# Kernel tuning notes

Measured on AMD Instinct MI355X. Metric: run time of the kernel, lower is better.

## Reference

```python
import jax, jax.numpy as jnp
import numpy as np

B, N, M, V, H, K = 32, 9, 128, 512, 256, 8
TYPES, PAD, TAU = 21, 0, 1.0
NS, NT = N - 1, TYPES - 9  # span slots (2..N), type slots (9..TYPES-1)


def setup_inputs() -> dict:
    key = jax.random.key(0)
    ks = jax.random.split(key, 6)
    decodings = jax.random.normal(ks[0], (B, N, M, V), jnp.float32)
    target_types = jax.random.randint(ks[1], (B,), 9, TYPES)
    spans = jax.random.randint(ks[2], (B,), 2, N + 1)
    type_emb = jax.random.normal(ks[3], (TYPES, H), jnp.float32)
    dec_sem_W = jax.random.normal(ks[4], (NS, NT, K * (N + 1), H), jnp.float32) / np.sqrt(H).astype(np.float32)
    dec_sem_b = jnp.zeros((NS, NT, K * (N + 1)), jnp.float32)
    u = jax.random.uniform(ks[5], (B, K, N + 1), jnp.float32, 1e-10, 1.0)
    gumbel = -jnp.log(-jnp.log(u))
    return dict(decodings=decodings, type_emb=type_emb, dec_sem_W=dec_sem_W,
                dec_sem_b=dec_sem_b, gumbel=gumbel,
                target_types=target_types, spans=spans)


def reference(decodings, type_emb, dec_sem_W, dec_sem_b, gumbel, target_types, spans):
    # --- per-sample template logits: decoder_sem[span-2][type-9](type_embedding) ---
    emb = type_emb[target_types]                           # (B, H)
    Wi = dec_sem_W[spans - 2, target_types - 9]            # (B, K*(N+1), H)
    bi = dec_sem_b[spans - 2, target_types - 9]            # (B, K*(N+1))
    logits = (jnp.einsum('boh,bh->bo', Wi, emb) + bi).reshape(B, K, N + 1)
    pos = jnp.arange(N + 1)
    valid = pos[None, None, :] <= spans[:, None, None]     # first span+1 slots only
    logits = jnp.where(valid, logits, -1e30)
    logp = jax.nn.log_softmax(logits, -1)
    # gumbel_softmax(hard=True), straight-through
    y_soft = jax.nn.softmax((logp + gumbel) / TAU, -1)
    y_hard = jax.nn.one_hot(jnp.argmax(y_soft, -1), N + 1, dtype=y_soft.dtype)
    dt = y_hard + y_soft - jax.lax.stop_gradient(y_soft)
    dt = jnp.where(valid, dt, 0.0)
    # type == 20 uses the fixed start template (row 0 picks decoding 0, rest pad)
    start = jnp.zeros((K, N + 1)).at[0, 1].set(1.0).at[1:, 0].set(1.0)
    dt = jnp.where((target_types == 20)[:, None, None], start[None], dt)

    # --- apply_decoder_template, vectorized over batch ---
    pad_row = jnp.tile(jax.nn.one_hot(PAD, V, dtype=decodings.dtype), M)  # (M*V,)
    pos_m = jnp.arange(M)

    def per_sample(dt_i, dec_i):
        choices = jnp.concatenate([pad_row[None], dec_i.reshape(N, M * V)], 0)  # (N+1, M*V)
        out = (dt_i @ choices).reshape(K, M, V)            # (K, M, V)
        idxs = jnp.argmax(out, -1)                         # (K, M)
        raw_len = jnp.max(jnp.where(idxs != PAD, pos_m + 1, 0), axis=1)  # (K,)
        ends = jnp.minimum(jnp.cumsum(raw_len), M)
        starts = jnp.concatenate([jnp.zeros(1, ends.dtype), ends[:-1]])
        lens = ends - starts                               # sequential clipped concat
        dest = starts[:, None] + pos_m[None]
        ok = pos_m[None] < lens[:, None]
        dest = jnp.where(ok, dest, M)                      # dump invalid writes in row M
        res = jnp.zeros((M + 1, V), out.dtype).at[dest.reshape(-1)].add(
            out.reshape(K * M, V) * ok.reshape(-1, 1))
        return res[:M]

    new_d = jax.vmap(per_sample)(dt, decodings)            # (B, M, V)
    new_v = jnp.zeros((B, 20, 3, V), decodings.dtype)
    return new_d, new_v
```

## Files before the change

### kernel.cpp

```cpp
#include <hip/hip_runtime.h>

#define B 32
#define N 9
#define M 128
#define V 512
#define H 256
#define K 8
#define NT 12
#define NP1 10
#define SPLITS 4
#define ROWS_PER_SPLIT 32
#define NEWV_ROWS (B*20*3)

__device__ __forceinline__ float wave_sum(float v) {
    #pragma unroll
    for (int off = 32; off > 0; off >>= 1) v += __shfl_xor(v, off, 64);
    return v;
}

__global__ __launch_bounds__(256) void k_sel_rawlen(
    const float* __restrict__ dec, const float* __restrict__ type_emb,
    const float* __restrict__ W, const float* __restrict__ bias,
    const float* __restrict__ gumbel, const int* __restrict__ types,
    const int* __restrict__ spans,
    int* __restrict__ jstar, int* __restrict__ part)
{
    const int blk = blockIdx.x;
    const int s  = blk & (SPLITS - 1);
    const int bk = blk >> 2;
    const int b  = bk >> 3, k = bk & 7;
    const int t = threadIdx.x, wave = t >> 6, lane = t & 63;

    __shared__ float logits_s[NP1];
    __shared__ int   j_s;
    __shared__ int   best_s[4];

    if (wave == 0) {
        const int typ  = types[b];
        const int span = spans[b];
        const long base = ((long)(span - 2) * NT + (typ - 9)) * (K * NP1) + k * NP1;
        const float e0 = type_emb[typ * H + lane      ];
        const float e1 = type_emb[typ * H + lane +  64];
        const float e2 = type_emb[typ * H + lane + 128];
        const float e3 = type_emb[typ * H + lane + 192];
        #pragma unroll
        for (int j = 0; j < NP1; ++j) {
            const float* w = W + (base + j) * H;
            float ssum = w[lane      ] * e0 + w[lane +  64] * e1
                       + w[lane + 128] * e2 + w[lane + 192] * e3;
            ssum = wave_sum(ssum);
            if (lane == 0) logits_s[j] = ssum;
        }
        if (lane == 0) {
            int bj = 0;
            if (typ == 20) {
                bj = (k == 0) ? 1 : 0;
            } else {
                float bestv = -3.0e38f;
                for (int j = 0; j <= span; ++j) {
                    float v = logits_s[j] + bias[base + j] + gumbel[bk * NP1 + j];
                    if (v > bestv) { bestv = v; bj = j; }
                }
            }
            j_s = bj;
        }
    }
    __syncthreads();
    const int j = j_s;
    if (t == 0) jstar[bk] = j;

    int best = 0;
    if (j > 0) {
        const float* src = dec + ((long)(b * N + (j - 1)) * M) * V;
        const int m0 = s * ROWS_PER_SPLIT + wave * 8;
        #pragma unroll
        for (int i = 0; i < 8; ++i) {
            const int m = m0 + i;
            const float4* row = (const float4*)(src + (long)m * V);
            float4 a = row[lane];
            float4 c = row[lane + 64];
            float x0 = __shfl(a.x, 0, 64);
            float loc = (lane == 0) ? fmaxf(fmaxf(a.y, a.z), a.w)
                                    : fmaxf(fmaxf(a.x, a.y), fmaxf(a.z, a.w));
            loc = fmaxf(loc, fmaxf(fmaxf(c.x, c.y), fmaxf(c.z, c.w)));
            if (__ballot(loc > x0)) best = m + 1;
        }
    }
    if (lane == 0) best_s[wave] = best;
    __syncthreads();
    if (t == 0)
        part[blk] = max(max(best_s[0], best_s[1]), max(best_s[2], best_s[3]));
}

__global__ __launch_bounds__(128) void k_write(
    const float* __restrict__ dec, const int* __restrict__ jstar,
    const int* __restrict__ part, float* __restrict__ out)
{
    const int blk = blockIdx.x;
    const int t = threadIdx.x;

    if (blk >= B * M) {
        const int r = blk - B * M;
        float4* dst = (float4*)(out + (long)B * M * V + (long)r * V);
        dst[t] = make_float4(0.f, 0.f, 0.f, 0.f);
        return;
    }

    const int b = blk >> 7, m = blk & 127;

    int found_k = -1, src_m = 0, cum = 0;
    #pragma unroll
    for (int k = 0; k < K; ++k) {
        const int* p = part + (b * K + k) * SPLITS;
        const int rl = max(max(p[0], p[1]), max(p[2], p[3]));
        const int e = min(cum + rl, M);
        if (found_k < 0 && m < e) { found_k = k; src_m = m - cum; }
        cum = e;
    }

    float4* dst = (float4*)(out + ((long)b * M + m) * V);
    if (found_k < 0) {
        dst[t] = make_float4(0.f, 0.f, 0.f, 0.f);
    } else {
        const int j = jstar[b * K + found_k];
        const float4* src = (const float4*)(dec + ((long)(b * N + (j - 1)) * M + src_m) * V);
        dst[t] = src[t];
    }
}

extern "C" void kernel_launch(void* const* d_in, const int* in_sizes, int n_in,
                              void* d_out, int out_size, void* d_ws, size_t ws_size,
                              hipStream_t stream) {
    const float* dec      = (const float*)d_in[0];
    const float* type_emb = (const float*)d_in[1];
    const float* W        = (const float*)d_in[2];
    const float* bias     = (const float*)d_in[3];
    const float* gumbel   = (const float*)d_in[4];
    const int*   types    = (const int*)d_in[5];
    const int*   spans    = (const int*)d_in[6];
    float* out = (float*)d_out;

    int* jstar = (int*)d_ws;
    int* part  = jstar + B * K;

    k_sel_rawlen<<<B * K * SPLITS, 256, 0, stream>>>(
        dec, type_emb, W, bias, gumbel, types, spans, jstar, part);
    k_write<<<B * M + NEWV_ROWS, 128, 0, stream>>>(dec, jstar, part, out);
}
```

Before: 126.4 us.

## Decouple slab scan from template selection and scan each decoding slab once

The first kernel now scans every (batch, decoding-slab) pair once, skipping slabs beyond the span, instead of scanning the selected slab per (batch, k). Template selection runs in separate blocks, with the logit dot products spread across waves using float4 loads. The write kernel looks up each raw length through jstar into the per-slab partial maxima, and it now copies two rows per 256-thread block. This cuts redundant reads when several k pick the same slab and removes the dependency between selection and scanning, but it may read slabs that no k selects.

```diff
diff --git a/kernel.cpp b/kernel.cpp
--- a/kernel.cpp
+++ b/kernel.cpp
@@ -8,8 +8,10 @@
 #define K 8
 #define NT 12
 #define NP1 10
-#define SPLITS 4
-#define ROWS_PER_SPLIT 32
+#define SPLITS 8
+#define ROWS_PER_SPLIT 16
+#define SCAN_BLKS (B*N*SPLITS)
+#define SEL_BLKS (B*K)
 #define NEWV_ROWS (B*20*3)
 
 __device__ __forceinline__ float wave_sum(float v) {
@@ -18,7 +20,7 @@
     return v;
 }
 
-__global__ __launch_bounds__(256) void k_sel_rawlen(
+__global__ __launch_bounds__(256) void k_scan_sel(
     const float* __restrict__ dec, const float* __restrict__ type_emb,
     const float* __restrict__ W, const float* __restrict__ bias,
     const float* __restrict__ gumbel, const int* __restrict__ types,
@@ -26,55 +28,21 @@
     int* __restrict__ jstar, int* __restrict__ part)
 {
     const int blk = blockIdx.x;
-    const int s  = blk & (SPLITS - 1);
-    const int bk = blk >> 2;
-    const int b  = bk >> 3, k = bk & 7;
     const int t = threadIdx.x, wave = t >> 6, lane = t & 63;
 
-    __shared__ float logits_s[NP1];
-    __shared__ int   j_s;
-    __shared__ int   best_s[4];
+    if (blk < SCAN_BLKS) {
+        const int s  = blk & (SPLITS - 1);
+        const int bs = blk >> 3;
+        const int b = bs / N, slab = bs % N;
+        const int typ = types[b], span = spans[b];
+        if (slab >= span) return;
+        if (typ == 20 && slab != 0) return;
 
-    if (wave == 0) {
-        const int typ  = types[b];
-        const int span = spans[b];
-        const long base = ((long)(span - 2) * NT + (typ - 9)) * (K * NP1) + k * NP1;
-        const float e0 = type_emb[typ * H + lane      ];
-        const float e1 = type_emb[typ * H + lane +  64];
-        const float e2 = type_emb[typ * H + lane + 128];
-        const float e3 = type_emb[typ * H + lane + 192];
+        const float* src = dec + (long)bs * M * V;
+        int best = 0;
+        const int m0 = s * ROWS_PER_SPLIT + wave * 4;
         #pragma unroll
-        for (int j = 0; j < NP1; ++j) {
-            const float* w = W + (base + j) * H;
-            float ssum = w[lane      ] * e0 + w[lane +  64] * e1
-                       + w[lane + 128] * e2 + w[lane + 192] * e3;
-            ssum = wave_sum(ssum);
-            if (lane == 0) logits_s[j] = ssum;
-        }
-        if (lane == 0) {
-            int bj = 0;
-            if (typ == 20) {
-                bj = (k == 0) ? 1 : 0;
-            } else {
-                float bestv = -3.0e38f;
-                for (int j = 0; j <= span; ++j) {
-                    float v = logits_s[j] + bias[base + j] + gumbel[bk * NP1 + j];
-                    if (v > bestv) { bestv = v; bj = j; }
-                }
-            }
-            j_s = bj;
-        }
-    }
-    __syncthreads();
-    const int j = j_s;
-    if (t == 0) jstar[bk] = j;
-
-    int best = 0;
-    if (j > 0) {
-        const float* src = dec + ((long)(b * N + (j - 1)) * M) * V;
-        const int m0 = s * ROWS_PER_SPLIT + wave * 8;
-        #pragma unroll
-        for (int i = 0; i < 8; ++i) {
+        for (int i = 0; i < 4; ++i) {
             const int m = m0 + i;
             const float4* row = (const float4*)(src + (long)m * V);
             float4 a = row[lane];
@@ -85,34 +53,71 @@
             loc = fmaxf(loc, fmaxf(fmaxf(c.x, c.y), fmaxf(c.z, c.w)));
             if (__ballot(loc > x0)) best = m + 1;
         }
+        __shared__ int bs_s[4];
+        if (lane == 0) bs_s[wave] = best;
+        __syncthreads();
+        if (t == 0)
+            part[blk] = max(max(bs_s[0], bs_s[1]), max(bs_s[2], bs_s[3]));
+    } else {
+        const int bk = blk - SCAN_BLKS;
+        const int b = bk >> 3, k = bk & 7;
+        const int typ = types[b], span = spans[b];
+        __shared__ float logits_s[NP1];
+
+        const long base = ((long)(span - 2) * NT + (typ - 9)) * (K * NP1) + k * NP1;
+        const float4 e4 = ((const float4*)(type_emb + typ * H))[lane];
+        for (int j = wave; j < NP1; j += 4) {
+            const float4 w4 = ((const float4*)(W + (base + j) * H))[lane];
+            float ssum = w4.x * e4.x + w4.y * e4.y + w4.z * e4.z + w4.w * e4.w;
+            ssum = wave_sum(ssum);
+            if (lane == 0)
+                logits_s[j] = ssum + bias[base + j] + gumbel[bk * NP1 + j];
+        }
+        __syncthreads();
+        if (t == 0) {
+            int bj = 0;
+            if (typ == 20) {
+                bj = (k == 0) ? 1 : 0;
+            } else {
+                float bestv = -3.0e38f;
+                for (int j = 0; j <= span; ++j) {
+                    const float v = logits_s[j];
+                    if (v > bestv) { bestv = v; bj = j; }
+                }
+            }
+            jstar[bk] = bj;
+        }
     }
-    if (lane == 0) best_s[wave] = best;
-    __syncthreads();
-    if (t == 0)
-        part[blk] = max(max(best_s[0], best_s[1]), max(best_s[2], best_s[3]));
 }
 
-__global__ __launch_bounds__(128) void k_write(
+__global__ __launch_bounds__(256) void k_write(
     const float* __restrict__ dec, const int* __restrict__ jstar,
     const int* __restrict__ part, float* __restrict__ out)
 {
     const int blk = blockIdx.x;
     const int t = threadIdx.x;
+    const int half = t >> 7, t1 = t & 127;
 
-    if (blk >= B * M) {
-        const int r = blk - B * M;
+    if (blk >= B * (M / 2)) {
+        const int r = (blk - B * (M / 2)) * 2 + half;
         float4* dst = (float4*)(out + (long)B * M * V + (long)r * V);
-        dst[t] = make_float4(0.f, 0.f, 0.f, 0.f);
+        dst[t1] = make_float4(0.f, 0.f, 0.f, 0.f);
         return;
     }
 
-    const int b = blk >> 7, m = blk & 127;
+    const int b = blk >> 6;
+    const int m = ((blk & 63) << 1) + half;
 
     int found_k = -1, src_m = 0, cum = 0;
     #pragma unroll
     for (int k = 0; k < K; ++k) {
-        const int* p = part + (b * K + k) * SPLITS;
-        const int rl = max(max(p[0], p[1]), max(p[2], p[3]));
+        const int j = jstar[b * K + k];
+        int rl = 0;
+        if (j > 0) {
+            const int* p = part + ((b * N + (j - 1)) << 3);
+            #pragma unroll
+            for (int q = 0; q < SPLITS; ++q) rl = max(rl, p[q]);
+        }
         const int e = min(cum + rl, M);
         if (found_k < 0 && m < e) { found_k = k; src_m = m - cum; }
         cum = e;
@@ -120,11 +125,11 @@
 
     float4* dst = (float4*)(out + ((long)b * M + m) * V);
     if (found_k < 0) {
-        dst[t] = make_float4(0.f, 0.f, 0.f, 0.f);
+        dst[t1] = make_float4(0.f, 0.f, 0.f, 0.f);
     } else {
         const int j = jstar[b * K + found_k];
         const float4* src = (const float4*)(dec + ((long)(b * N + (j - 1)) * M + src_m) * V);
-        dst[t] = src[t];
+        dst[t1] = src[t1];
     }
 }
 
@@ -143,7 +148,7 @@
     int* jstar = (int*)d_ws;
     int* part  = jstar + B * K;
 
-    k_sel_rawlen<<<B * K * SPLITS, 256, 0, stream>>>(
+    k_scan_sel<<<SCAN_BLKS + SEL_BLKS, 256, 0, stream>>>(
         dec, type_emb, W, bias, gumbel, types, spans, jstar, part);
-    k_write<<<B * M + NEWV_ROWS, 128, 0, stream>>>(dec, jstar, part, out);
+    k_write<<<B * (M / 2) + NEWV_ROWS / 2, 256, 0, stream>>>(dec, jstar, part, out);
 }
```

New measurement: 123.0 us. -2.7%, faster.
